# Performance work log

Hardware: AMD Instinct MI355X
Metric: run time of the kernel (lower is better)

## Reference

```python
import jax, jax.numpy as jnp
import numpy as np

N = 50000
E = 640000
F_IN = 128
HID = 128
OUT = 64


def setup_inputs() -> dict:
    key = jax.random.key(0)
    ks = jax.random.split(key, 16)
    x = jax.random.normal(ks[0], (N, F_IN), dtype=jnp.float32)
    edge_index = jax.random.randint(ks[1], (2, E), 0, N, dtype=jnp.int64)

    def lin(k, fan_in, fan_out):
        bound = 1.0 / np.sqrt(fan_in)
        kw, kb = jax.random.split(k)
        W = jax.random.uniform(kw, (fan_in, fan_out), jnp.float32, -bound, bound)
        b = jax.random.uniform(kb, (fan_out,), jnp.float32, -bound, bound)
        return W, b

    W1, b1 = lin(ks[2], F_IN, HID)
    W2, b2 = lin(ks[3], HID, HID)
    W3, b3 = lin(ks[4], HID, HID)
    Wres, bres = lin(ks[5], F_IN, HID)
    Wlin, blin = lin(ks[6], HID, OUT)
    return {"x": x, "edge_index": edge_index,
            "W1": W1, "b1": b1, "W2": W2, "b2": b2, "W3": W3, "b3": b3,
            "Wres": Wres, "bres": bres, "Wlin": Wlin, "blin": blin}


def _gcn_norm(edge_index, n):
    # GCNConv default: add self-loops, symmetric normalization D^-1/2 (A+I) D^-1/2
    src, dst = edge_index[0], edge_index[1]
    deg = jax.ops.segment_sum(jnp.ones((edge_index.shape[1],), jnp.float32), dst,
                              num_segments=n) + 1.0  # +1 for self-loop
    dinv = jax.lax.rsqrt(deg)
    norm_e = dinv[src] * dinv[dst]          # [E] edge coefficients
    norm_self = 1.0 / deg                    # [N] self-loop coefficients
    return src, dst, norm_e, norm_self


def _gcn_conv(x, W, b, src, dst, norm_e, norm_self, n):
    h = x @ W                                # [N, F_out]
    agg = jax.ops.segment_sum(h[src] * norm_e[:, None], dst, num_segments=n)
    agg = agg + h * norm_self[:, None]       # self-loop contribution
    return agg + b


def reference(x, edge_index, W1, b1, W2, b2, W3, b3, Wres, bres, Wlin, blin):
    n = x.shape[0]
    src, dst, norm_e, norm_self = _gcn_norm(edge_index, n)
    x_res = x @ Wres + bres
    h = _gcn_conv(x, W1, b1, src, dst, norm_e, norm_self, n)
    h = jax.nn.relu(h + x_res)               # dropout is identity in eval mode
    h = _gcn_conv(h, W2, b2, src, dst, norm_e, norm_self, n)
    h = jax.nn.relu(h)
    h = _gcn_conv(h, W3, b3, src, dst, norm_e, norm_self, n)
    h = jax.nn.relu(h)
    return h @ Wlin + blin
```

## Files before the change

kernel.cpp:

```cpp
#include <hip/hip_runtime.h>

typedef unsigned short ushort_t;
typedef unsigned int uint_t;

typedef __bf16 bf16x8 __attribute__((ext_vector_type(8)));
typedef float f32x4 __attribute__((ext_vector_type(4)));

union BFU { ushort_t u; __bf16 h; };

__device__ __forceinline__ float bf2f(uint_t u) {
    union { uint_t i; float f; } v; v.i = u << 16; return v.f;
}
__device__ __forceinline__ ushort_t f2bf(float f) {
    union { float f; uint_t i; } v; v.f = f;
    uint_t r = v.i + 0x7fffu + ((v.i >> 16) & 1u);
    return (ushort_t)(r >> 16);
}
__device__ __forceinline__ float loadF(const void* p, size_t i, int isBf16) {
    return isBf16 ? bf2f((uint_t)((const ushort_t*)p)[i]) : ((const float*)p)[i];
}

struct DetectArgs {
    const void* t[11];
    int elems[11];
    const int* ei;
    int* flags;
};

__global__ void k_init(DetectArgs a, int* __restrict__ deg, int n) {
    int i = blockIdx.x * blockDim.x + threadIdx.x;
    if (i < n) deg[i] = 0;
    if (blockIdx.x == 0) {
        int t = threadIdx.x;
        if (t < 11) {
            const uint_t* w = (const uint_t*)a.t[t];
            int m = a.elems[t] / 2; if (m > 64) m = 64;
            int cnt = 0;
            for (int k = 0; k < m; ++k) {
                uint_t field = (w[k] >> 7) & 0xFFu;
                cnt += (field >= 100u && field <= 135u);
            }
            a.flags[t] = (cnt * 10 >= m * 6) ? 1 : 0;
        } else if (t == 11) {
            int nz = 0;
            for (int k = 0; k < 64; ++k) nz += (a.ei[2 * k + 1] != 0);
            a.flags[11] = (nz == 0) ? 1 : 0;
        }
    }
}

__global__ void k_deg(const int* __restrict__ ei, int E, int N,
                      const int* __restrict__ flags, int* __restrict__ deg,
                      int2* __restrict__ tmp) {
    int i = blockIdx.x * blockDim.x + threadIdx.x;
    int e0 = i * 4;
    if (e0 >= E) return;
    int is64 = flags[11];
    if (e0 + 3 < E && (E & 3) == 0) {
        int d[4];
        if (is64) {
            int4 va = *(const int4*)(ei + 2 * E + 2 * e0);
            int4 vb = *(const int4*)(ei + 2 * E + 2 * e0 + 4);
            d[0] = va.x; d[1] = va.z; d[2] = vb.x; d[3] = vb.z;
        } else {
            int4 va = *(const int4*)(ei + E + e0);
            d[0] = va.x; d[1] = va.y; d[2] = va.z; d[3] = va.w;
        }
        int l[4]; bool ok[4];
#pragma unroll
        for (int k = 0; k < 4; ++k) ok[k] = (unsigned)d[k] < (unsigned)N;
#pragma unroll
        for (int k = 0; k < 4; ++k)
            l[k] = ok[k] ? atomicAdd(&deg[d[k]], 1) : 0;
        int4 t01, t23;
        t01.x = ok[0] ? d[0] : -1; t01.y = l[0];
        t01.z = ok[1] ? d[1] : -1; t01.w = l[1];
        t23.x = ok[2] ? d[2] : -1; t23.y = l[2];
        t23.z = ok[3] ? d[3] : -1; t23.w = l[3];
        *(int4*)(tmp + e0) = t01;
        *(int4*)(tmp + e0 + 2) = t23;
    } else {
        for (int e = e0; e < E && e < e0 + 4; ++e) {
            int dd = is64 ? ei[2 * E + 2 * e] : ei[E + e];
            bool ok = (unsigned)dd < (unsigned)N;
            int l = ok ? atomicAdd(&deg[dd], 1) : 0;
            tmp[e] = make_int2(ok ? dd : -1, l);
        }
    }
}


__global__ __launch_bounds__(256) void k_bsum(const int* __restrict__ deg, int n,
                                              int* __restrict__ bsum) {
    int base = blockIdx.x * 1024;
    int local = 0;
#pragma unroll
    for (int j = 0; j < 4; ++j) {
        int idx = base + threadIdx.x + j * 256;
        if (idx < n) local += deg[idx];
    }
    __shared__ int s[4];
#pragma unroll
    for (int off = 32; off; off >>= 1) local += __shfl_down(local, off, 64);
    if ((threadIdx.x & 63) == 0) s[threadIdx.x >> 6] = local;
    __syncthreads();
    if (threadIdx.x == 0) bsum[blockIdx.x] = s[0] + s[1] + s[2] + s[3];
}

__global__ __launch_bounds__(256) void k_bscan(int* __restrict__ bsum, int nb) {
    __shared__ int s[256];
    int t = threadIdx.x;
    int v = (t < nb) ? bsum[t] : 0;
    s[t] = v;
    __syncthreads();
    for (int off = 1; off < 256; off <<= 1) {
        int u = (t >= off) ? s[t - off] : 0;
        __syncthreads();
        s[t] += u;
        __syncthreads();
    }
    if (t < nb) bsum[t] = s[t] - v;
}

__global__ __launch_bounds__(256) void k_rowptr(const int* __restrict__ deg,
                                                const int* __restrict__ boff, int n,
                                                int* __restrict__ row_ptr,
                                                float* __restrict__ dinv,
                                                float* __restrict__ nself) {
    __shared__ int s[256];
    int t = threadIdx.x;
    int base = blockIdx.x * 1024 + t * 4;
    int v0 = (base + 0 < n) ? deg[base + 0] : 0;
    int v1 = (base + 1 < n) ? deg[base + 1] : 0;
    int v2 = (base + 2 < n) ? deg[base + 2] : 0;
    int v3 = (base + 3 < n) ? deg[base + 3] : 0;
    int tot = v0 + v1 + v2 + v3;
    s[t] = tot;
    __syncthreads();
    for (int off = 1; off < 256; off <<= 1) {
        int u = (t >= off) ? s[t - off] : 0;
        __syncthreads();
        s[t] += u;
        __syncthreads();
    }
    int run = boff[blockIdx.x] + ((t == 0) ? 0 : s[t - 1]);
    int vals[4] = {v0, v1, v2, v3};
#pragma unroll
    for (int j = 0; j < 4; ++j) {
        int idx = base + j;
        if (idx < n) {
            row_ptr[idx] = run;
            run += vals[j];
            float df = (float)vals[j] + 1.0f;
            dinv[idx] = rsqrtf(df);
            nself[idx] = 1.0f / df;
        }
    }
    if (blockIdx.x == gridDim.x - 1 && t == 255) row_ptr[n] = boff[blockIdx.x] + s[255];
}

__global__ void k_scatter(const int* __restrict__ ei, int E, int N,
                          const int* __restrict__ flags,
                          const int* __restrict__ row_ptr,
                          const float* __restrict__ dinv,
                          const int2* __restrict__ tmp,
                          uint2* __restrict__ colwgt) {
    int i = blockIdx.x * blockDim.x + threadIdx.x;
    int e0 = i * 4;
    if (e0 >= E) return;
    int is64 = flags[11];
    if (e0 + 3 < E && (E & 3) == 0) {
        int s[4];
        if (is64) {
            int4 sa = *(const int4*)(ei + 2 * e0);
            int4 sb = *(const int4*)(ei + 2 * e0 + 4);
            s[0] = sa.x; s[1] = sa.z; s[2] = sb.x; s[3] = sb.z;
        } else {
            int4 sa = *(const int4*)(ei + e0);
            s[0] = sa.x; s[1] = sa.y; s[2] = sa.z; s[3] = sa.w;
        }
        int4 t01 = *(const int4*)(tmp + e0);
        int4 t23 = *(const int4*)(tmp + e0 + 2);
        int d[4] = {t01.x, t01.z, t23.x, t23.z};
        int l[4] = {t01.y, t01.w, t23.y, t23.w};
        int ss[4]; int pos[4]; float wv[4];
#pragma unroll
        for (int k = 0; k < 4; ++k)
            ss[k] = ((unsigned)s[k] < (unsigned)N) ? s[k] : 0;
#pragma unroll
        for (int k = 0; k < 4; ++k) {
            if (d[k] >= 0) {
                pos[k] = row_ptr[d[k]] + l[k];
                wv[k] = dinv[ss[k]] * dinv[d[k]];
            }
        }
#pragma unroll
        for (int k = 0; k < 4; ++k) {
            if (d[k] >= 0) {
                uint2 pk;
                pk.x = (uint_t)ss[k];
                pk.y = __float_as_uint(wv[k]);
                colwgt[pos[k]] = pk;
            }
        }
    } else {
        for (int e = e0; e < E && e < e0 + 4; ++e) {
            int sv = is64 ? ei[2 * e] : ei[e];
            int2 tv = tmp[e];
            if (tv.x >= 0) {
                int ssv = ((unsigned)sv < (unsigned)N) ? sv : 0;
                uint2 pk;
                pk.x = (uint_t)ssv;
                pk.y = __float_as_uint(dinv[ssv] * dinv[tv.x]);
                colwgt[row_ptr[tv.x] + tv.y] = pk;
            }
        }
    }
}

__global__ void k_pack(const void* __restrict__ W1, const void* __restrict__ W2,
                       const void* __restrict__ W3, const void* __restrict__ Wr,
                       const void* __restrict__ Wl, const int* __restrict__ flags,
                       ushort_t* __restrict__ Tcat, ushort_t* __restrict__ T2,
                       ushort_t* __restrict__ T3, ushort_t* __restrict__ Tl) {
    int i = blockIdx.x * blockDim.x + threadIdx.x;
    const int SQ = 128 * 128;
    if (i < 4 * SQ) {
        int m = i / SQ, r = i % SQ;
        int k = r / 128, f = r % 128;
        const void* W = (m == 0) ? W1 : (m == 1) ? W2 : (m == 2) ? W3 : Wr;
        int fid = (m == 0) ? 1 : (m == 1) ? 3 : (m == 2) ? 5 : 7;
        ushort_t* T = (m == 0) ? Tcat : (m == 1) ? T2 : (m == 2) ? T3 : (Tcat + SQ);
        T[f * 128 + k] = f2bf(loadF(W, (size_t)k * 128 + f, flags[fid]));
    } else if (i < 4 * SQ + 128 * 64) {
        int r = i - 4 * SQ;
        int k = r / 64, f = r % 64;
        Tl[f * 128 + k] = f2bf(loadF(Wl, (size_t)k * 64 + f, flags[9]));
    }
}


template <int NCT>
__device__ __forceinline__ void stage_B(const ushort_t* __restrict__ WT, uint4* lds) {
    int t = threadIdx.x;
#pragma unroll
    for (int i = 0; i < NCT; ++i) {
        int g = i * 256 + t;
        uint4 v = ((const uint4*)WT)[g];
        int col = g >> 4, k8 = g & 15;
        int c = col >> 4, l16c = col & 15;
        int kk = k8 >> 2, q = k8 & 3;
        lds[((kk * NCT + c) << 6) + (q << 4) + l16c] = v;
    }
    __syncthreads();
}

__device__ __forceinline__ void load_A2(const void* __restrict__ A, int a16,
                                        int ar0, int ar1, int quad,
                                        bf16x8 afrag[2][4]) {
    if (a16) {
        const ushort_t* p0 = (const ushort_t*)A + (size_t)ar0 * 128 + quad * 8;
        const ushort_t* p1 = (const ushort_t*)A + (size_t)ar1 * 128 + quad * 8;
#pragma unroll
        for (int kk = 0; kk < 4; ++kk) {
            afrag[0][kk] = *(const bf16x8*)(p0 + kk * 32);
            afrag[1][kk] = *(const bf16x8*)(p1 + kk * 32);
        }
    } else {
        const float* p0 = (const float*)A + (size_t)ar0 * 128 + quad * 8;
        const float* p1 = (const float*)A + (size_t)ar1 * 128 + quad * 8;
#pragma unroll
        for (int kk = 0; kk < 4; ++kk) {
            f32x4 u0 = *(const f32x4*)(p0 + kk * 32);
            f32x4 u1 = *(const f32x4*)(p0 + kk * 32 + 4);
            f32x4 v0 = *(const f32x4*)(p1 + kk * 32);
            f32x4 v1 = *(const f32x4*)(p1 + kk * 32 + 4);
#pragma unroll
            for (int j = 0; j < 4; ++j) {
                BFU e;
                e.u = f2bf(u0[j]); afrag[0][kk][j] = e.h;
                e.u = f2bf(u1[j]); afrag[0][kk][j + 4] = e.h;
                e.u = f2bf(v0[j]); afrag[1][kk][j] = e.h;
                e.u = f2bf(v1[j]); afrag[1][kk][j + 4] = e.h;
            }
        }
    }
}

template <int NCT>
__global__ __launch_bounds__(256, 2) void k_gemm2(const void* __restrict__ A, int aFid, int aFix,
                                                  const ushort_t* __restrict__ WT,
                                                  const void* __restrict__ bias, int bFid,
                                                  void* __restrict__ C, int cFix,
                                                  int M, const int* __restrict__ flags) {
    __shared__ uint4 lds[NCT * 256];
    stage_B<NCT>(WT, lds);

    const int F = NCT * 16;
    int t = threadIdx.x;
    int wave = t >> 6, lane = t & 63;
    int quad = lane >> 4, l16 = lane & 15;
    int rowBase = blockIdx.x * 128 + wave * 32;

    int a16 = (aFid >= 0) ? flags[aFid] : aFix;
    int ar0 = rowBase + l16;      if (ar0 >= M) ar0 = M - 1;
    int ar1 = rowBase + 16 + l16; if (ar1 >= M) ar1 = M - 1;

    bf16x8 afrag[2][4];
    load_A2(A, a16, ar0, ar1, quad, afrag);

    f32x4 acc[2][NCT];
#pragma unroll
    for (int r = 0; r < 2; ++r)
#pragma unroll
        for (int c = 0; c < NCT; ++c) acc[r][c] = (f32x4){0.f, 0.f, 0.f, 0.f};

#pragma unroll
    for (int kk = 0; kk < 4; ++kk) {
#pragma unroll
        for (int c = 0; c < NCT; ++c) {
            bf16x8 b = *(const bf16x8*)&lds[((kk * NCT + c) << 6) + lane];
            acc[0][c] = __builtin_amdgcn_mfma_f32_16x16x32_bf16(afrag[0][kk], b, acc[0][c], 0, 0, 0);
            acc[1][c] = __builtin_amdgcn_mfma_f32_16x16x32_bf16(afrag[1][kk], b, acc[1][c], 0, 0, 0);
        }
    }

    int bf = (bias && bFid >= 0) ? flags[bFid] : 1;
#pragma unroll
    for (int r = 0; r < 2; ++r) {
#pragma unroll
        for (int c = 0; c < NCT; ++c) {
            int colg = c * 16 + l16;
            float bv = bias ? loadF(bias, colg, bf) : 0.0f;
#pragma unroll
            for (int q = 0; q < 4; ++q) {
                int row = rowBase + r * 16 + quad * 4 + q;
                if (row < M) {
                    float v = acc[r][c][q] + bv;
                    if (cFix) ((ushort_t*)C)[(size_t)row * F + colg] = f2bf(v);
                    else      ((float*)C)[(size_t)row * F + colg] = v;
                }
            }
        }
    }
}

__global__ __launch_bounds__(256, 1) void k_gemm_l1(const void* __restrict__ A,
                                                    const ushort_t* __restrict__ Tcat,
                                                    const void* __restrict__ bres,
                                                    ushort_t* __restrict__ Hout,
                                                    ushort_t* __restrict__ Xres,
                                                    int M, const int* __restrict__ flags) {
    __shared__ uint4 lds[16 * 256];
    stage_B<16>(Tcat, lds);

    int t = threadIdx.x;
    int wave = t >> 6, lane = t & 63;
    int quad = lane >> 4, l16 = lane & 15;
    int rowBase = blockIdx.x * 128 + wave * 32;

    int a16 = flags[0];
    int ar0 = rowBase + l16;      if (ar0 >= M) ar0 = M - 1;
    int ar1 = rowBase + 16 + l16; if (ar1 >= M) ar1 = M - 1;

    bf16x8 afrag[2][4];
    load_A2(A, a16, ar0, ar1, quad, afrag);

    f32x4 acc[2][16];
#pragma unroll
    for (int r = 0; r < 2; ++r)
#pragma unroll
        for (int c = 0; c < 16; ++c) acc[r][c] = (f32x4){0.f, 0.f, 0.f, 0.f};

#pragma unroll
    for (int kk = 0; kk < 4; ++kk) {
#pragma unroll
        for (int c = 0; c < 16; ++c) {
            bf16x8 b = *(const bf16x8*)&lds[((kk * 16 + c) << 6) + lane];
            acc[0][c] = __builtin_amdgcn_mfma_f32_16x16x32_bf16(afrag[0][kk], b, acc[0][c], 0, 0, 0);
            acc[1][c] = __builtin_amdgcn_mfma_f32_16x16x32_bf16(afrag[1][kk], b, acc[1][c], 0, 0, 0);
        }
    }

    int bf = flags[8];
#pragma unroll
    for (int r = 0; r < 2; ++r) {
#pragma unroll
        for (int c = 0; c < 16; ++c) {
            int colg = c * 16 + l16;
            float bv = (c >= 8) ? loadF(bres, colg - 128, bf) : 0.0f;
#pragma unroll
            for (int q = 0; q < 4; ++q) {
                int row = rowBase + r * 16 + quad * 4 + q;
                if (row < M) {
                    float v = acc[r][c][q] + bv;
                    if (c < 8) Hout[(size_t)row * 128 + colg] = f2bf(v);
                    else       Xres[(size_t)row * 128 + (colg - 128)] = f2bf(v);
                }
            }
        }
    }
}

__global__ __launch_bounds__(256) void k_agg(const ushort_t* __restrict__ H,
                                             const int* __restrict__ row_ptr,
                                             const uint2* __restrict__ colwgt,
                                             const float* __restrict__ nself,
                                             const void* __restrict__ bias, int bFid,
                                             const ushort_t* __restrict__ other,
                                             ushort_t* __restrict__ Out,
                                             int n, const int* __restrict__ flags) {
    int node = (blockIdx.x * blockDim.x + threadIdx.x) >> 6;
    if (node >= n) return;
    int lane = threadIdx.x & 63;
    int f = lane * 2;

    float ns = nself[node];
    size_t nidx = (size_t)node * 128 + f;

    uint_t hv = *(const uint_t*)(H + nidx);
    float a0 = bf2f(hv & 0xffffu) * ns;
    float a1 = bf2f(hv >> 16) * ns;

    int beg = row_ptr[node], end = row_ptr[node + 1];
    for (int bs = beg; bs < end; bs += 64) {
        int rem = end - bs;
        int nb = (rem < 64) ? rem : 64;
        uint2 m = (lane < nb) ? colwgt[bs + lane] : (uint2){0u, 0u};
        int c = (int)m.x;
        float w = __uint_as_float(m.y);

        for (int j = 0; j < nb; j += 16) {
            int si[16]; float wi[16]; uint_t vi[16];
#pragma unroll
            for (int q = 0; q < 16; ++q) {
                si[q] = __shfl(c, j + q, 64);
                wi[q] = __shfl(w, j + q, 64);
            }
#pragma unroll
            for (int q = 0; q < 16; ++q)
                vi[q] = *(const uint_t*)(H + (size_t)si[q] * 128 + f);
#pragma unroll
            for (int q = 0; q < 16; ++q) {
                a0 = fmaf(bf2f(vi[q] & 0xffffu), wi[q], a0);
                a1 = fmaf(bf2f(vi[q] >> 16), wi[q], a1);
            }
        }
    }

    int bfm = flags[bFid];
    a0 += loadF(bias, f, bfm);
    a1 += loadF(bias, f + 1, bfm);
    if (other) {
        uint_t ov = *(const uint_t*)(other + nidx);
        a0 += bf2f(ov & 0xffffu);
        a1 += bf2f(ov >> 16);
    }
    a0 = fmaxf(a0, 0.0f);
    a1 = fmaxf(a1, 0.0f);
    uint_t outv = (uint_t)f2bf(a0) | ((uint_t)f2bf(a1) << 16);
    *(uint_t*)(Out + nidx) = outv;
}


extern "C" void kernel_launch(void* const* d_in, const int* in_sizes, int n_in,
                              void* d_out, int out_size, void* d_ws, size_t ws_size,
                              hipStream_t stream) {
    const int N = in_sizes[0] / 128;
    const int E = in_sizes[1] / 2;

    const void* x  = d_in[0];
    const int*  ei = (const int*)d_in[1];

    char* ws = (char*)d_ws;
    size_t used = 0;
    auto alloc = [&](size_t bytes) {
        char* p = ws + used;
        used += (bytes + 255) & ~(size_t)255;
        return p;
    };

    int*   flags   = (int*)alloc(64 * 4);
    int*   deg     = (int*)alloc((size_t)N * 4);
    int*   row_ptr = (int*)alloc((size_t)(N + 1) * 4);
    float* dinv    = (float*)alloc((size_t)N * 4);
    float* nself   = (float*)alloc((size_t)N * 4);
    int2*  tmp     = (int2*)alloc((size_t)E * 8);
    uint2* colwgt  = (uint2*)alloc((size_t)E * 8);
    int*   bsum    = (int*)alloc(256 * 4);
    ushort_t* Tcat = (ushort_t*)alloc(256 * 128 * 2);
    ushort_t* T2   = (ushort_t*)alloc(128 * 128 * 2);
    ushort_t* T3   = (ushort_t*)alloc(128 * 128 * 2);
    ushort_t* Tlin = (ushort_t*)alloc(128 * 64 * 2);

    ushort_t* Hbuf = (ushort_t*)alloc((size_t)N * 128 * 2);
    ushort_t* Act1 = (ushort_t*)alloc((size_t)N * 128 * 2);
    ushort_t* Act2 = (ushort_t*)alloc((size_t)N * 128 * 2);
    ushort_t* Xres = (ushort_t*)alloc((size_t)N * 128 * 2);

    if (used > ws_size) return;

    DetectArgs da;
    for (int i = 0; i < 11; ++i) { da.t[i] = d_in[i == 0 ? 0 : i + 1]; da.elems[i] = in_sizes[i == 0 ? 0 : i + 1]; }
    da.ei = ei;
    da.flags = flags;

    const int B = 256;
    int gInit = (N + B - 1) / B;
    int gE4   = ((E + 3) / 4 + B - 1) / B;
    int gPack = (4 * 128 * 128 + 128 * 64 + B - 1) / B;
    int gGemm = (N + 127) / 128;
    int gAgg  = (N + 3) / 4;
    int nb    = (N + 1023) / 1024;

    k_init<<<gInit, B, 0, stream>>>(da, deg, N);
    k_pack<<<gPack, B, 0, stream>>>(d_in[2], d_in[4], d_in[6], d_in[8], d_in[10], flags,
                                    Tcat, T2, T3, Tlin);
    k_deg<<<gE4, B, 0, stream>>>(ei, E, N, flags, deg, tmp);
    k_bsum<<<nb, B, 0, stream>>>(deg, N, bsum);
    k_bscan<<<1, B, 0, stream>>>(bsum, nb);
    k_rowptr<<<nb, B, 0, stream>>>(deg, bsum, N, row_ptr, dinv, nself);
    k_scatter<<<gE4, B, 0, stream>>>(ei, E, N, flags, row_ptr, dinv, tmp, colwgt);

    k_gemm_l1<<<gGemm, B, 0, stream>>>(x, Tcat, d_in[9], Hbuf, Xres, N, flags);
    k_agg<<<gAgg, B, 0, stream>>>(Hbuf, row_ptr, colwgt, nself, d_in[3], 2,
                                  Xres, Act1, N, flags);

    k_gemm2<8><<<gGemm, B, 0, stream>>>(Act1, -1, 1, T2, nullptr, -1, Hbuf, 1, N, flags);
    k_agg<<<gAgg, B, 0, stream>>>(Hbuf, row_ptr, colwgt, nself, d_in[5], 4,
                                  nullptr, Act2, N, flags);

    k_gemm2<8><<<gGemm, B, 0, stream>>>(Act2, -1, 1, T3, nullptr, -1, Hbuf, 1, N, flags);
    k_agg<<<gAgg, B, 0, stream>>>(Hbuf, row_ptr, colwgt, nself, d_in[7], 6,
                                  nullptr, Act1, N, flags);

    k_gemm2<4><<<gGemm, B, 0, stream>>>(Act1, -1, 1, Tlin, d_in[11], 10,
                                        d_out, 0, N, flags);
}
```

Before: 331.7 us.

## Halve GEMM row tiles for occupancy and merge dtype detection into weight packing

```diff
diff --git a/kernel.cpp b/kernel.cpp
--- a/kernel.cpp
+++ b/kernel.cpp
@@ -27,25 +27,49 @@
     int* flags;
 };
 
-__global__ void k_init(DetectArgs a, int* __restrict__ deg, int n) {
+__device__ __forceinline__ int detect_one(const void* p, int elems) {
+    const uint_t* w = (const uint_t*)p;
+    int n = elems / 2; if (n > 64) n = 64;
+    int cnt = 0;
+    for (int k = 0; k < n; ++k) {
+        uint_t f = (w[k] >> 7) & 0xFFu;
+        cnt += (f >= 100u && f <= 135u);
+    }
+    return (cnt * 10 >= n * 6) ? 1 : 0;
+}
+
+__global__ void k_pack(DetectArgs a,
+                       ushort_t* __restrict__ Tcat, ushort_t* __restrict__ T2,
+                       ushort_t* __restrict__ T3, ushort_t* __restrict__ Tl) {
+    __shared__ int lflag;
     int i = blockIdx.x * blockDim.x + threadIdx.x;
-    if (i < n) deg[i] = 0;
-    if (blockIdx.x == 0) {
-        int t = threadIdx.x;
-        if (t < 11) {
-            const uint_t* w = (const uint_t*)a.t[t];
-            int m = a.elems[t] / 2; if (m > 64) m = 64;
-            int cnt = 0;
-            for (int k = 0; k < m; ++k) {
-                uint_t field = (w[k] >> 7) & 0xFFu;
-                cnt += (field >= 100u && field <= 135u);
-            }
-            a.flags[t] = (cnt * 10 >= m * 6) ? 1 : 0;
-        } else if (t == 11) {
-            int nz = 0;
-            for (int k = 0; k < 64; ++k) nz += (a.ei[2 * k + 1] != 0);
-            a.flags[11] = (nz == 0) ? 1 : 0;
-        }
+    const int SQ = 128 * 128;
+    int m = (i < 4 * SQ) ? (i / SQ) : 4;
+    int fid = (m == 0) ? 1 : (m == 1) ? 3 : (m == 2) ? 5 : (m == 3) ? 7 : 9;
+    const void* W = a.t[fid];
+
+    if (threadIdx.x == 0) lflag = detect_one(W, a.elems[fid]);
+    if (blockIdx.x == 0 && threadIdx.x >= 64 && threadIdx.x < 75) {
+        int t = threadIdx.x - 64;
+        a.flags[t] = detect_one(a.t[t], a.elems[t]);
+    }
+    if (blockIdx.x == 0 && threadIdx.x == 75) {
+        int nz = 0;
+        for (int k = 0; k < 64; ++k) nz += (a.ei[2 * k + 1] != 0);
+        a.flags[11] = (nz == 0) ? 1 : 0;
+    }
+    __syncthreads();
+    int isb = lflag;
+
+    if (i < 4 * SQ) {
+        int r = i % SQ;
+        int k = r / 128, f = r % 128;
+        ushort_t* T = (m == 0) ? Tcat : (m == 1) ? T2 : (m == 2) ? T3 : (Tcat + SQ);
+        T[f * 128 + k] = f2bf(loadF(W, (size_t)k * 128 + f, isb));
+    } else if (i < 4 * SQ + 128 * 64) {
+        int r = i - 4 * SQ;
+        int k = r / 64, f = r % 64;
+        Tl[f * 128 + k] = f2bf(loadF(W, (size_t)k * 64 + f, isb));
     }
 }
 
@@ -218,27 +242,6 @@
     }
 }
 
-__global__ void k_pack(const void* __restrict__ W1, const void* __restrict__ W2,
-                       const void* __restrict__ W3, const void* __restrict__ Wr,
-                       const void* __restrict__ Wl, const int* __restrict__ flags,
-                       ushort_t* __restrict__ Tcat, ushort_t* __restrict__ T2,
-                       ushort_t* __restrict__ T3, ushort_t* __restrict__ Tl) {
-    int i = blockIdx.x * blockDim.x + threadIdx.x;
-    const int SQ = 128 * 128;
-    if (i < 4 * SQ) {
-        int m = i / SQ, r = i % SQ;
-        int k = r / 128, f = r % 128;
-        const void* W = (m == 0) ? W1 : (m == 1) ? W2 : (m == 2) ? W3 : Wr;
-        int fid = (m == 0) ? 1 : (m == 1) ? 3 : (m == 2) ? 5 : 7;
-        ushort_t* T = (m == 0) ? Tcat : (m == 1) ? T2 : (m == 2) ? T3 : (Tcat + SQ);
-        T[f * 128 + k] = f2bf(loadF(W, (size_t)k * 128 + f, flags[fid]));
-    } else if (i < 4 * SQ + 128 * 64) {
-        int r = i - 4 * SQ;
-        int k = r / 64, f = r % 64;
-        Tl[f * 128 + k] = f2bf(loadF(Wl, (size_t)k * 64 + f, flags[9]));
-    }
-}
-
 
 template <int NCT>
 __device__ __forceinline__ void stage_B(const ushort_t* __restrict__ WT, uint4* lds) {
@@ -255,40 +258,30 @@
     __syncthreads();
 }
 
-__device__ __forceinline__ void load_A2(const void* __restrict__ A, int a16,
-                                        int ar0, int ar1, int quad,
-                                        bf16x8 afrag[2][4]) {
+__device__ __forceinline__ void load_A1(const void* __restrict__ A, int a16,
+                                        int ar, int quad, bf16x8 af[4]) {
     if (a16) {
-        const ushort_t* p0 = (const ushort_t*)A + (size_t)ar0 * 128 + quad * 8;
-        const ushort_t* p1 = (const ushort_t*)A + (size_t)ar1 * 128 + quad * 8;
+        const ushort_t* p = (const ushort_t*)A + (size_t)ar * 128 + quad * 8;
+#pragma unroll
+        for (int kk = 0; kk < 4; ++kk) af[kk] = *(const bf16x8*)(p + kk * 32);
+    } else {
+        const float* p = (const float*)A + (size_t)ar * 128 + quad * 8;
 #pragma unroll
         for (int kk = 0; kk < 4; ++kk) {
-            afrag[0][kk] = *(const bf16x8*)(p0 + kk * 32);
-            afrag[1][kk] = *(const bf16x8*)(p1 + kk * 32);
-        }
-    } else {
-        const float* p0 = (const float*)A + (size_t)ar0 * 128 + quad * 8;
-        const float* p1 = (const float*)A + (size_t)ar1 * 128 + quad * 8;
-#pragma unroll
-        for (int kk = 0; kk < 4; ++kk) {
-            f32x4 u0 = *(const f32x4*)(p0 + kk * 32);
-            f32x4 u1 = *(const f32x4*)(p0 + kk * 32 + 4);
-            f32x4 v0 = *(const f32x4*)(p1 + kk * 32);
-            f32x4 v1 = *(const f32x4*)(p1 + kk * 32 + 4);
+            f32x4 u0 = *(const f32x4*)(p + kk * 32);
+            f32x4 u1 = *(const f32x4*)(p + kk * 32 + 4);
 #pragma unroll
             for (int j = 0; j < 4; ++j) {
                 BFU e;
-                e.u = f2bf(u0[j]); afrag[0][kk][j] = e.h;
-                e.u = f2bf(u1[j]); afrag[0][kk][j + 4] = e.h;
-                e.u = f2bf(v0[j]); afrag[1][kk][j] = e.h;
-                e.u = f2bf(v1[j]); afrag[1][kk][j + 4] = e.h;
+                e.u = f2bf(u0[j]); af[kk][j] = e.h;
+                e.u = f2bf(u1[j]); af[kk][j + 4] = e.h;
             }
         }
     }
 }
 
 template <int NCT>
-__global__ __launch_bounds__(256, 2) void k_gemm2(const void* __restrict__ A, int aFid, int aFix,
+__global__ __launch_bounds__(256, 4) void k_gemm2(const void* __restrict__ A, int aFid, int aFix,
                                                   const ushort_t* __restrict__ WT,
                                                   const void* __restrict__ bias, int bFid,
                                                   void* __restrict__ C, int cFix,
@@ -300,103 +293,109 @@
     int t = threadIdx.x;
     int wave = t >> 6, lane = t & 63;
     int quad = lane >> 4, l16 = lane & 15;
-    int rowBase = blockIdx.x * 128 + wave * 32;
+    int row0 = blockIdx.x * 64 + wave * 16;
 
     int a16 = (aFid >= 0) ? flags[aFid] : aFix;
-    int ar0 = rowBase + l16;      if (ar0 >= M) ar0 = M - 1;
-    int ar1 = rowBase + 16 + l16; if (ar1 >= M) ar1 = M - 1;
-
-    bf16x8 afrag[2][4];
-    load_A2(A, a16, ar0, ar1, quad, afrag);
-
-    f32x4 acc[2][NCT];
-#pragma unroll
-    for (int r = 0; r < 2; ++r)
-#pragma unroll
-        for (int c = 0; c < NCT; ++c) acc[r][c] = (f32x4){0.f, 0.f, 0.f, 0.f};
+    int ar = row0 + l16; if (ar >= M) ar = M - 1;
+
+    bf16x8 af[4];
+    load_A1(A, a16, ar, quad, af);
+
+    f32x4 acc[NCT];
+#pragma unroll
+    for (int c = 0; c < NCT; ++c) acc[c] = (f32x4){0.f, 0.f, 0.f, 0.f};
 
 #pragma unroll
     for (int kk = 0; kk < 4; ++kk) {
 #pragma unroll
         for (int c = 0; c < NCT; ++c) {
             bf16x8 b = *(const bf16x8*)&lds[((kk * NCT + c) << 6) + lane];
-            acc[0][c] = __builtin_amdgcn_mfma_f32_16x16x32_bf16(afrag[0][kk], b, acc[0][c], 0, 0, 0);
-            acc[1][c] = __builtin_amdgcn_mfma_f32_16x16x32_bf16(afrag[1][kk], b, acc[1][c], 0, 0, 0);
+            acc[c] = __builtin_amdgcn_mfma_f32_16x16x32_bf16(af[kk], b, acc[c], 0, 0, 0);
         }
     }
 
     int bf = (bias && bFid >= 0) ? flags[bFid] : 1;
 #pragma unroll
-    for (int r = 0; r < 2; ++r) {
-#pragma unroll
-        for (int c = 0; c < NCT; ++c) {
-            int colg = c * 16 + l16;
-            float bv = bias ? loadF(bias, colg, bf) : 0.0f;
-#pragma unroll
-            for (int q = 0; q < 4; ++q) {
-                int row = rowBase + r * 16 + quad * 4 + q;
-                if (row < M) {
-                    float v = acc[r][c][q] + bv;
-                    if (cFix) ((ushort_t*)C)[(size_t)row * F + colg] = f2bf(v);
-                    else      ((float*)C)[(size_t)row * F + colg] = v;
-                }
-            }
-        }
-    }
-}
-
-__global__ __launch_bounds__(256, 1) void k_gemm_l1(const void* __restrict__ A,
+    for (int c = 0; c < NCT; ++c) {
+        int colg = c * 16 + l16;
+        float bv = bias ? loadF(bias, colg, bf) : 0.0f;
+#pragma unroll
+        for (int q = 0; q < 4; ++q) {
+            int row = row0 + quad * 4 + q;
+            if (row < M) {
+                float v = acc[c][q] + bv;
+                if (cFix) ((ushort_t*)C)[(size_t)row * F + colg] = f2bf(v);
+                else      ((float*)C)[(size_t)row * F + colg] = v;
+            }
+        }
+    }
+}
+
+__global__ __launch_bounds__(256, 4) void k_gemm_l1(const void* __restrict__ A,
                                                     const ushort_t* __restrict__ Tcat,
                                                     const void* __restrict__ bres,
                                                     ushort_t* __restrict__ Hout,
                                                     ushort_t* __restrict__ Xres,
                                                     int M, const int* __restrict__ flags) {
-    __shared__ uint4 lds[16 * 256];
-    stage_B<16>(Tcat, lds);
-
+    __shared__ uint4 lds[8 * 256];
     int t = threadIdx.x;
     int wave = t >> 6, lane = t & 63;
     int quad = lane >> 4, l16 = lane & 15;
-    int rowBase = blockIdx.x * 128 + wave * 32;
+    int row0 = blockIdx.x * 64 + wave * 16;
 
     int a16 = flags[0];
-    int ar0 = rowBase + l16;      if (ar0 >= M) ar0 = M - 1;
-    int ar1 = rowBase + 16 + l16; if (ar1 >= M) ar1 = M - 1;
-
-    bf16x8 afrag[2][4];
-    load_A2(A, a16, ar0, ar1, quad, afrag);
-
-    f32x4 acc[2][16];
-#pragma unroll
-    for (int r = 0; r < 2; ++r)
-#pragma unroll
-        for (int c = 0; c < 16; ++c) acc[r][c] = (f32x4){0.f, 0.f, 0.f, 0.f};
-
-#pragma unroll
-    for (int kk = 0; kk < 4; ++kk) {
-#pragma unroll
-        for (int c = 0; c < 16; ++c) {
-            bf16x8 b = *(const bf16x8*)&lds[((kk * 16 + c) << 6) + lane];
-            acc[0][c] = __builtin_amdgcn_mfma_f32_16x16x32_bf16(afrag[0][kk], b, acc[0][c], 0, 0, 0);
-            acc[1][c] = __builtin_amdgcn_mfma_f32_16x16x32_bf16(afrag[1][kk], b, acc[1][c], 0, 0, 0);
-        }
-    }
-
-    int bf = flags[8];
-#pragma unroll
-    for (int r = 0; r < 2; ++r) {
-#pragma unroll
-        for (int c = 0; c < 16; ++c) {
+    int ar = row0 + l16; if (ar >= M) ar = M - 1;
+
+    bf16x8 af[4];
+    load_A1(A, a16, ar, quad, af);
+
+    stage_B<8>(Tcat, lds);
+    {
+        f32x4 acc[8];
+#pragma unroll
+        for (int c = 0; c < 8; ++c) acc[c] = (f32x4){0.f, 0.f, 0.f, 0.f};
+#pragma unroll
+        for (int kk = 0; kk < 4; ++kk) {
+#pragma unroll
+            for (int c = 0; c < 8; ++c) {
+                bf16x8 b = *(const bf16x8*)&lds[((kk * 8 + c) << 6) + lane];
+                acc[c] = __builtin_amdgcn_mfma_f32_16x16x32_bf16(af[kk], b, acc[c], 0, 0, 0);
+            }
+        }
+#pragma unroll
+        for (int c = 0; c < 8; ++c) {
             int colg = c * 16 + l16;
-            float bv = (c >= 8) ? loadF(bres, colg - 128, bf) : 0.0f;
 #pragma unroll
             for (int q = 0; q < 4; ++q) {
-                int row = rowBase + r * 16 + quad * 4 + q;
-                if (row < M) {
-                    float v = acc[r][c][q] + bv;
-                    if (c < 8) Hout[(size_t)row * 128 + colg] = f2bf(v);
-                    else       Xres[(size_t)row * 128 + (colg - 128)] = f2bf(v);
-                }
+                int row = row0 + quad * 4 + q;
+                if (row < M) Hout[(size_t)row * 128 + colg] = f2bf(acc[c][q]);
+            }
+        }
+    }
+    __syncthreads();
+
+    stage_B<8>(Tcat + 128 * 128, lds);
+    {
+        int bf = flags[8];
+        f32x4 acc[8];
+#pragma unroll
+        for (int c = 0; c < 8; ++c) acc[c] = (f32x4){0.f, 0.f, 0.f, 0.f};
+#pragma unroll
+        for (int kk = 0; kk < 4; ++kk) {
+#pragma unroll
+            for (int c = 0; c < 8; ++c) {
+                bf16x8 b = *(const bf16x8*)&lds[((kk * 8 + c) << 6) + lane];
+                acc[c] = __builtin_amdgcn_mfma_f32_16x16x32_bf16(af[kk], b, acc[c], 0, 0, 0);
+            }
+        }
+#pragma unroll
+        for (int c = 0; c < 8; ++c) {
+            int colg = c * 16 + l16;
+            float bv = loadF(bres, colg, bf);
+#pragma unroll
+            for (int q = 0; q < 4; ++q) {
+                int row = row0 + quad * 4 + q;
+                if (row < M) Xres[(size_t)row * 128 + colg] = f2bf(acc[c][q] + bv);
             }
         }
     }
@@ -506,16 +505,14 @@
     da.flags = flags;
 
     const int B = 256;
-    int gInit = (N + B - 1) / B;
     int gE4   = ((E + 3) / 4 + B - 1) / B;
-    int gPack = (4 * 128 * 128 + 128 * 64 + B - 1) / B;
-    int gGemm = (N + 127) / 128;
+    int gPack = (4 * 128 * 128 + 128 * 64) / B;
+    int gGemm = (N + 63) / 64;
     int gAgg  = (N + 3) / 4;
     int nb    = (N + 1023) / 1024;
 
-    k_init<<<gInit, B, 0, stream>>>(da, deg, N);
-    k_pack<<<gPack, B, 0, stream>>>(d_in[2], d_in[4], d_in[6], d_in[8], d_in[10], flags,
-                                    Tcat, T2, T3, Tlin);
+    hipMemsetAsync(deg, 0, (size_t)N * 4, stream);
+    k_pack<<<gPack, B, 0, stream>>>(da, Tcat, T2, T3, Tlin);
     k_deg<<<gE4, B, 0, stream>>>(ei, E, N, flags, deg, tmp);
     k_bsum<<<nb, B, 0, stream>>>(deg, N, bsum);
     k_bscan<<<1, B, 0, stream>>>(bsum, nb);
```

Measured after the change: 305.7 us. 7.8% less time.
